# Performance work log

Measured on AMD Instinct MI355X. Metric: run time of the kernel, lower is better.

Reference implementation:

```python
import jax, jax.numpy as jnp
import numpy as np

N, E, DIN, DOUT = 10000, 160000, 256, 256
NEG_SLOPE = 0.2
BN_EPS = 1e-5
DROP_P = 0.5


def setup_inputs() -> dict:
    key = jax.random.key(0)
    ks = jax.random.split(key, 12)
    s = 1.0 / np.sqrt(DIN)
    return {
        "x": jax.random.normal(ks[0], (N, DIN), jnp.float32),
        "edge_index": jax.random.randint(ks[1], (2, E), 0, N, jnp.int64),
        "Wl": jax.random.normal(ks[2], (DIN, DOUT), jnp.float32) * s,
        "bl": jax.random.normal(ks[3], (DOUT,), jnp.float32) * s,
        "Wr": jax.random.normal(ks[4], (DIN, DOUT), jnp.float32) * s,
        "br": jax.random.normal(ks[5], (DOUT,), jnp.float32) * s,
        "att": jax.random.normal(ks[6], (DOUT,), jnp.float32) * (1.0 / np.sqrt(DOUT)),
        "bias": jax.random.normal(ks[7], (DOUT,), jnp.float32) * 0.01,
        "gamma": jnp.ones((DOUT,), jnp.float32),
        "beta": jnp.zeros((DOUT,), jnp.float32),
        "dropout_u": jax.random.uniform(ks[8], (N, DOUT), jnp.float32),
    }


def reference(x, edge_index, Wl, bl, Wr, br, att, bias, gamma, beta, dropout_u):
    n = x.shape[0]
    # GATv2Conv (heads=1): separate source/target linear maps
    xl = x @ Wl + bl  # source features [N, DOUT]
    xr = x @ Wr + br  # target features [N, DOUT]
    # add self-loops (PyG default add_self_loops=True)
    loop = jnp.arange(n, dtype=edge_index.dtype)
    src = jnp.concatenate([edge_index[0], loop])  # [E+N]
    dst = jnp.concatenate([edge_index[1], loop])
    # GATv2 attention: e = att . LeakyReLU(xl_j + xr_i)
    h = jax.nn.leaky_relu(xl[src] + xr[dst], NEG_SLOPE)  # [E+N, DOUT]
    alpha = h @ att  # [E+N]
    # segment softmax over destination nodes
    amax = jax.ops.segment_max(alpha, dst, num_segments=n)
    alpha = jnp.exp(alpha - amax[dst])
    denom = jax.ops.segment_sum(alpha, dst, num_segments=n)
    alpha = alpha / denom[dst]
    # scatter-add aggregate of weighted source features
    out = jax.ops.segment_sum(xl[src] * alpha[:, None], dst, num_segments=n)
    out = out + bias
    # ReLU -> dropout(p=0.5, training) -> BatchNorm (training stats)
    out = jax.nn.relu(out)
    mask = (dropout_u >= DROP_P).astype(out.dtype) / (1.0 - DROP_P)
    out = out * mask
    mean = out.mean(axis=0)
    var = out.var(axis=0)  # biased, as BatchNorm uses for normalization
    out = gamma * (out - mean) * jax.lax.rsqrt(var + BN_EPS) + beta
    return out
```

## Files before the change

kernel.cpp:

```cpp
#include <hip/hip_runtime.h>
#include <hip/hip_bf16.h>
#include <math.h>

#define D 256
#define CAP 128
#define NEG_SLOPE 0.2f
#define BN_EPS 1e-5f

typedef __attribute__((ext_vector_type(8))) short bf16x8;
typedef __attribute__((ext_vector_type(8))) unsigned short ushort8;
typedef __attribute__((ext_vector_type(4))) float f32x4;

__device__ inline unsigned short f2bf(float f) {
    union { float f; unsigned u; } v; v.f = f;
    unsigned u = v.u;
    unsigned r = u + 0x7FFFu + ((u >> 16) & 1u);
    return (unsigned short)(r >> 16);
}
__device__ inline float bf2f(unsigned short u) {
    union { unsigned u; float f; } v; v.u = ((unsigned)u) << 16; return v.f;
}

__global__ void prep_kernel(const float* __restrict__ Wl, const float* __restrict__ Wr,
                            int* __restrict__ zero_base, int nzero,
                            unsigned short* __restrict__ Bt) {
    int b = blockIdx.x;
    if (b < 42) {
        int idx = b * 256 + threadIdx.x;
        if (idx < nzero) zero_base[idx] = 0;
    } else {
        int n = b - 42;
        int k = threadIdx.x;
        const float* W = (n < 256) ? Wl : Wr;
        int nn = n & 255;
        Bt[(size_t)n * 256 + k] = f2bf(W[(size_t)k * 256 + nn]);
    }
}

__global__ __launch_bounds__(256) void gemm_scatter_kernel(
    const float* __restrict__ X, const unsigned short* __restrict__ Bt,
    const float* __restrict__ bl, const float* __restrict__ br,
    const int* __restrict__ ei, int* __restrict__ counts, int* __restrict__ ssrc,
    unsigned short* __restrict__ xlbf, float* __restrict__ xr,
    int M, int E, int N, int ngemm)
{
    if ((int)blockIdx.x >= ngemm) {
        int e = (blockIdx.x - ngemm) * 256 + threadIdx.x;
        if (e < E + N) {
            int src, dst;
            if (e < E) { src = ei[e]; dst = ei[E + e]; }
            else       { src = dst = e - E; }
            int pos = atomicAdd(&counts[dst], 1);
            if (pos < CAP) ssrc[dst * CAP + pos] = src;
        }
        return;
    }

    __shared__ __align__(16) unsigned short As[64][136];
    __shared__ __align__(16) unsigned short Bs[64][136];

    const int tid = threadIdx.x;
    const int wave = tid >> 6, lane = tid & 63;
    const int m_l = lane & 15, quad = lane >> 4;
    const int row0 = (blockIdx.x >> 3) * 64;
    const int n0 = (blockIdx.x & 7) * 64;

    f32x4 acc[4] = {};

    for (int k0 = 0; k0 < 256; k0 += 128) {
        __syncthreads();
        #pragma unroll
        for (int i = 0; i < 4; i++) {
            int c = tid + i * 256;
            int r = c >> 4;
            int u = (c & 15) * 8;
            int grow = row0 + r;
            ushort8 av = {0, 0, 0, 0, 0, 0, 0, 0};
            if (grow < M) {
                float4 f0 = *(const float4*)(X + (size_t)grow * 256 + k0 + u);
                float4 f1 = *(const float4*)(X + (size_t)grow * 256 + k0 + u + 4);
                av[0] = f2bf(f0.x); av[1] = f2bf(f0.y);
                av[2] = f2bf(f0.z); av[3] = f2bf(f0.w);
                av[4] = f2bf(f1.x); av[5] = f2bf(f1.y);
                av[6] = f2bf(f1.z); av[7] = f2bf(f1.w);
            }
            *(ushort8*)&As[r][u] = av;
            *(ushort8*)&Bs[r][u] = *(const ushort8*)(Bt + (size_t)(n0 + r) * 256 + k0 + u);
        }
        __syncthreads();

        #pragma unroll
        for (int kk0 = 0; kk0 < 128; kk0 += 32) {
            bf16x8 a = *(const bf16x8*)&As[wave * 16 + m_l][kk0 + quad * 8];
            #pragma unroll
            for (int c = 0; c < 4; c++) {
                bf16x8 b = *(const bf16x8*)&Bs[c * 16 + m_l][kk0 + quad * 8];
                acc[c] = __builtin_amdgcn_mfma_f32_16x16x32_bf16(a, b, acc[c], 0, 0, 0);
            }
        }
    }

    const bool isl = (n0 < 256);
    #pragma unroll
    for (int c = 0; c < 4; c++) {
        int col = n0 + c * 16 + m_l;
        int cc = col & 255;
        float bv = isl ? bl[cc] : br[cc];
        #pragma unroll
        for (int r = 0; r < 4; r++) {
            int row = row0 + wave * 16 + quad * 4 + r;
            if (row < M) {
                float v = acc[c][r] + bv;
                if (isl) xlbf[(size_t)row * 256 + cc] = f2bf(v);
                else     xr[(size_t)row * 256 + cc] = v;
            }
        }
    }
}

__device__ inline float dot8leaky(const float* f, float4 bA, float4 bB,
                                  float4 aA, float4 aB) {
    float h, s = 0.f;
    h = f[0] + bA.x; h = (h > 0.f) ? h : NEG_SLOPE * h; s += h * aA.x;
    h = f[1] + bA.y; h = (h > 0.f) ? h : NEG_SLOPE * h; s += h * aA.y;
    h = f[2] + bA.z; h = (h > 0.f) ? h : NEG_SLOPE * h; s += h * aA.z;
    h = f[3] + bA.w; h = (h > 0.f) ? h : NEG_SLOPE * h; s += h * aA.w;
    h = f[4] + bB.x; h = (h > 0.f) ? h : NEG_SLOPE * h; s += h * aB.x;
    h = f[5] + bB.y; h = (h > 0.f) ? h : NEG_SLOPE * h; s += h * aB.y;
    h = f[6] + bB.z; h = (h > 0.f) ? h : NEG_SLOPE * h; s += h * aB.z;
    h = f[7] + bB.w; h = (h > 0.f) ? h : NEG_SLOPE * h; s += h * aB.w;
    return s;
}

__global__ __launch_bounds__(256) void node_kernel(
    const unsigned short* __restrict__ xlbf, const float* __restrict__ xr,
    const float* __restrict__ att, const float* __restrict__ bias,
    const float* __restrict__ du, const int* __restrict__ counts,
    const int* __restrict__ ssrc, float* __restrict__ out, int N)
{
    const int wave = threadIdx.x >> 6, lane = threadIdx.x & 63;
    const int i = blockIdx.x * 4 + wave;
    if (i >= N) return;
    const int hl = lane & 31;
    const int sid = lane >> 5;

    const float4 attA = ((const float4*)att)[hl * 2];
    const float4 attB = ((const float4*)att)[hl * 2 + 1];
    const float4 bA = ((const float4*)(xr + (size_t)i * D))[hl * 2];
    const float4 bB = ((const float4*)(xr + (size_t)i * D))[hl * 2 + 1];

    int cnt = counts[i];
    if (cnt > CAP) cnt = CAP;
    const int start = i * CAP, end = start + cnt;

    float m = -INFINITY, lsum = 0.f;
    float acc[8] = {0.f, 0.f, 0.f, 0.f, 0.f, 0.f, 0.f, 0.f};
    const ushort8 z8 = {0, 0, 0, 0, 0, 0, 0, 0};

    int e = start + sid;
    ushort8 p0, p1, p2, p3;
    p0 = (e     < end) ? *(const ushort8*)(xlbf + (size_t)ssrc[e]     * D + hl * 8) : z8;
    p1 = (e + 2 < end) ? *(const ushort8*)(xlbf + (size_t)ssrc[e + 2] * D + hl * 8) : z8;
    p2 = (e + 4 < end) ? *(const ushort8*)(xlbf + (size_t)ssrc[e + 4] * D + hl * 8) : z8;
    p3 = (e + 6 < end) ? *(const ushort8*)(xlbf + (size_t)ssrc[e + 6] * D + hl * 8) : z8;

    while (e < end) {
        ushort8 c0 = p0, c1 = p1, c2 = p2, c3 = p3;
        bool v1 = (e + 2 < end), v2 = (e + 4 < end), v3 = (e + 6 < end);
        int en = e + 8;
        p0 = (en     < end) ? *(const ushort8*)(xlbf + (size_t)ssrc[en]     * D + hl * 8) : z8;
        p1 = (en + 2 < end) ? *(const ushort8*)(xlbf + (size_t)ssrc[en + 2] * D + hl * 8) : z8;
        p2 = (en + 4 < end) ? *(const ushort8*)(xlbf + (size_t)ssrc[en + 4] * D + hl * 8) : z8;
        p3 = (en + 6 < end) ? *(const ushort8*)(xlbf + (size_t)ssrc[en + 6] * D + hl * 8) : z8;

        float f0[8], f1[8], f2[8], f3[8];
        #pragma unroll
        for (int k = 0; k < 8; k++) {
            f0[k] = bf2f(c0[k]); f1[k] = bf2f(c1[k]);
            f2[k] = bf2f(c2[k]); f3[k] = bf2f(c3[k]);
        }

        float s0 = dot8leaky(f0, bA, bB, attA, attB);
        float s1 = dot8leaky(f1, bA, bB, attA, attB);
        float s2 = dot8leaky(f2, bA, bB, attA, attB);
        float s3 = dot8leaky(f3, bA, bB, attA, attB);

        #pragma unroll
        for (int off = 1; off < 32; off <<= 1) {
            s0 += __shfl_xor(s0, off);
            s1 += __shfl_xor(s1, off);
            s2 += __shfl_xor(s2, off);
            s3 += __shfl_xor(s3, off);
        }
        if (!v1) s1 = -INFINITY;
        if (!v2) s2 = -INFINITY;
        if (!v3) s3 = -INFINITY;

        float mnew = fmaxf(fmaxf(m, fmaxf(s0, s1)), fmaxf(s2, s3));
        float sc = __expf(m - mnew);
        float e0e = __expf(s0 - mnew);
        float e1e = __expf(s1 - mnew);
        float e2e = __expf(s2 - mnew);
        float e3e = __expf(s3 - mnew);
        lsum = lsum * sc + e0e + e1e + e2e + e3e;
        #pragma unroll
        for (int k = 0; k < 8; k++) {
            acc[k] = acc[k] * sc + e0e * f0[k] + e1e * f1[k]
                                 + e2e * f2[k] + e3e * f3[k];
        }
        m = mnew;
        e = en;
    }

    {
        float mO = __shfl_xor(m, 32);
        float lO = __shfl_xor(lsum, 32);
        float accO[8];
        #pragma unroll
        for (int k = 0; k < 8; k++) accO[k] = __shfl_xor(acc[k], 32);
        float mn = fmaxf(m, mO);
        float wS = (m  == -INFINITY) ? 0.f : __expf(m - mn);
        float wO = (mO == -INFINITY) ? 0.f : __expf(mO - mn);
        lsum = lsum * wS + lO * wO;
        #pragma unroll
        for (int k = 0; k < 8; k++) acc[k] = acc[k] * wS + accO[k] * wO;
    }

    if (lane < 32) {
        float inv = 1.f / lsum;
        float4 biA = ((const float4*)bias)[hl * 2];
        float4 biB = ((const float4*)bias)[hl * 2 + 1];
        float4 uA = ((const float4*)(du + (size_t)i * D))[hl * 2];
        float4 uB = ((const float4*)(du + (size_t)i * D))[hl * 2 + 1];
        float4 oA, oB;
        oA.x = fmaxf(acc[0] * inv + biA.x, 0.f); oA.x = (uA.x >= 0.5f) ? 2.f * oA.x : 0.f;
        oA.y = fmaxf(acc[1] * inv + biA.y, 0.f); oA.y = (uA.y >= 0.5f) ? 2.f * oA.y : 0.f;
        oA.z = fmaxf(acc[2] * inv + biA.z, 0.f); oA.z = (uA.z >= 0.5f) ? 2.f * oA.z : 0.f;
        oA.w = fmaxf(acc[3] * inv + biA.w, 0.f); oA.w = (uA.w >= 0.5f) ? 2.f * oA.w : 0.f;
        oB.x = fmaxf(acc[4] * inv + biB.x, 0.f); oB.x = (uB.x >= 0.5f) ? 2.f * oB.x : 0.f;
        oB.y = fmaxf(acc[5] * inv + biB.y, 0.f); oB.y = (uB.y >= 0.5f) ? 2.f * oB.y : 0.f;
        oB.z = fmaxf(acc[6] * inv + biB.z, 0.f); oB.z = (uB.z >= 0.5f) ? 2.f * oB.z : 0.f;
        oB.w = fmaxf(acc[7] * inv + biB.w, 0.f); oB.w = (uB.w >= 0.5f) ? 2.f * oB.w : 0.f;
        ((float4*)(out + (size_t)i * D))[hl * 2] = oA;
        ((float4*)(out + (size_t)i * D))[hl * 2 + 1] = oB;
    }
}

__global__ void bn_reduce_kernel(const float* __restrict__ pre,
                                 float* __restrict__ colsum,
                                 float* __restrict__ colsumsq, int N) {
    int t = threadIdx.x;
    float s = 0.f, s2 = 0.f;
    for (int r = blockIdx.x; r < N; r += gridDim.x) {
        float v = pre[(size_t)r * D + t];
        s += v; s2 += v * v;
    }
    atomicAdd(&colsum[t], s);
    atomicAdd(&colsumsq[t], s2);
}

__global__ void bn_apply_kernel(float* __restrict__ out,
                                const float* __restrict__ colsum,
                                const float* __restrict__ colsumsq,
                                const float* __restrict__ gamma,
                                const float* __restrict__ beta, int N) {
    int idx4 = blockIdx.x * 256 + threadIdx.x;
    int t0 = (idx4 * 4) & (D - 1);
    float invN = 1.f / (float)N;
    float4 v = ((const float4*)out)[idx4];
    float4 o;
    #pragma unroll
    for (int j = 0; j < 4; j++) {
        float mean = colsum[t0 + j] * invN;
        float var = colsumsq[t0 + j] * invN - mean * mean;
        float r = rsqrtf(var + BN_EPS);
        float vv = (j == 0) ? v.x : (j == 1) ? v.y : (j == 2) ? v.z : v.w;
        float oo = gamma[t0 + j] * (vv - mean) * r + beta[t0 + j];
        if (j == 0) o.x = oo; else if (j == 1) o.y = oo; else if (j == 2) o.z = oo; else o.w = oo;
    }
    ((float4*)out)[idx4] = o;
}

extern "C" void kernel_launch(void* const* d_in, const int* in_sizes, int n_in,
                              void* d_out, int out_size, void* d_ws, size_t ws_size,
                              hipStream_t stream) {
    const float* x     = (const float*)d_in[0];
    const int*   ei    = (const int*)d_in[1];
    const float* Wl    = (const float*)d_in[2];
    const float* bl    = (const float*)d_in[3];
    const float* Wr    = (const float*)d_in[4];
    const float* br    = (const float*)d_in[5];
    const float* att   = (const float*)d_in[6];
    const float* bias  = (const float*)d_in[7];
    const float* gamma = (const float*)d_in[8];
    const float* beta  = (const float*)d_in[9];
    const float* du    = (const float*)d_in[10];

    const int N = in_sizes[0] / D;
    const int E = in_sizes[1] / 2;

    int* ws = (int*)d_ws;
    size_t off = 0;
    float* xr       = (float*)(ws + off); off += (size_t)N * D;
    unsigned short* xlbf = (unsigned short*)(ws + off); off += (size_t)N * D / 2;
    unsigned short* Bt   = (unsigned short*)(ws + off); off += 512 * 256 / 2;
    int*   ssrc     = ws + off;           off += (size_t)N * CAP;
    float* colsum   = (float*)(ws + off); off += D;
    float* colsumsq = (float*)(ws + off); off += D;
    int*   counts   = ws + off;           off += N;
    int nzero = 2 * D + N;

    prep_kernel<<<42 + 512, 256, 0, stream>>>(Wl, Wr, (int*)colsum, nzero, Bt);

    int nMtiles = (N + 63) / 64;
    int ngemm = nMtiles * 8;
    int nscat = (E + N + 255) / 256;
    gemm_scatter_kernel<<<ngemm + nscat, 256, 0, stream>>>(
        x, Bt, bl, br, ei, counts, ssrc, xlbf, xr, N, E, N, ngemm);

    node_kernel<<<(N + 3) / 4, 256, 0, stream>>>(
        xlbf, xr, att, bias, du, counts, ssrc, (float*)d_out, N);

    bn_reduce_kernel<<<256, 256, 0, stream>>>((const float*)d_out, colsum, colsumsq, N);
    bn_apply_kernel<<<(N * D / 4 + 255) / 256, 256, 0, stream>>>(
        (float*)d_out, colsum, colsumsq, gamma, beta, N);
}
```

Before: 167.6 us.

## Pre-convert X to swizzled bf16 and load GEMM tiles directly into LDS

```diff
diff --git a/kernel.cpp b/kernel.cpp
--- a/kernel.cpp
+++ b/kernel.cpp
@@ -21,24 +21,50 @@
     union { unsigned u; float f; } v; v.u = ((unsigned)u) << 16; return v.f;
 }
 
-__global__ void prep_kernel(const float* __restrict__ Wl, const float* __restrict__ Wr,
+__device__ __forceinline__ void gload16(const void* g, void* l) {
+    __builtin_amdgcn_global_load_lds(
+        (const __attribute__((address_space(1))) unsigned int*)g,
+        (__attribute__((address_space(3))) unsigned int*)l,
+        16, 0, 0);
+}
+
+__global__ void prep_kernel(const float* __restrict__ X,
+                            const float* __restrict__ Wl, const float* __restrict__ Wr,
                             int* __restrict__ zero_base, int nzero,
-                            unsigned short* __restrict__ Bt) {
+                            unsigned short* __restrict__ Bt,
+                            unsigned short* __restrict__ Xbf, int N) {
     int b = blockIdx.x;
     if (b < 42) {
         int idx = b * 256 + threadIdx.x;
         if (idx < nzero) zero_base[idx] = 0;
-    } else {
+    } else if (b < 42 + 512) {
         int n = b - 42;
         int k = threadIdx.x;
         const float* W = (n < 256) ? Wl : Wr;
         int nn = n & 255;
-        Bt[(size_t)n * 256 + k] = f2bf(W[(size_t)k * 256 + nn]);
+        int ks = k ^ ((n & 7) << 3);
+        Bt[(size_t)n * 256 + ks] = f2bf(W[(size_t)k * 256 + nn]);
+    } else {
+        int idx = (b - 554) * 256 + threadIdx.x;
+        int row = idx >> 5;
+        int k0 = (idx & 31) * 8;
+        int ks = k0 ^ ((row & 7) << 3);
+        ushort8 v = {0, 0, 0, 0, 0, 0, 0, 0};
+        if (row < N) {
+            const float* src = X + (size_t)row * 256 + k0;
+            float4 f0 = *(const float4*)(src);
+            float4 f1 = *(const float4*)(src + 4);
+            v[0] = f2bf(f0.x); v[1] = f2bf(f0.y);
+            v[2] = f2bf(f0.z); v[3] = f2bf(f0.w);
+            v[4] = f2bf(f1.x); v[5] = f2bf(f1.y);
+            v[6] = f2bf(f1.z); v[7] = f2bf(f1.w);
+        }
+        *(ushort8*)(Xbf + (size_t)row * 256 + ks) = v;
     }
 }
 
 __global__ __launch_bounds__(256) void gemm_scatter_kernel(
-    const float* __restrict__ X, const unsigned short* __restrict__ Bt,
+    const unsigned short* __restrict__ Xbf, const unsigned short* __restrict__ Bt,
     const float* __restrict__ bl, const float* __restrict__ br,
     const int* __restrict__ ei, int* __restrict__ counts, int* __restrict__ ssrc,
     unsigned short* __restrict__ xlbf, float* __restrict__ xr,
@@ -56,14 +82,15 @@
         return;
     }
 
-    __shared__ __align__(16) unsigned short As[64][136];
-    __shared__ __align__(16) unsigned short Bs[64][136];
+    __shared__ __align__(16) unsigned short As[64 * 128];
+    __shared__ __align__(16) unsigned short Bs[64 * 128];
 
     const int tid = threadIdx.x;
     const int wave = tid >> 6, lane = tid & 63;
     const int m_l = lane & 15, quad = lane >> 4;
     const int row0 = (blockIdx.x >> 3) * 64;
     const int n0 = (blockIdx.x & 7) * 64;
+    const int sw = (m_l & 7) << 3;
 
     f32x4 acc[4] = {};
 
@@ -71,30 +98,23 @@
         __syncthreads();
         #pragma unroll
         for (int i = 0; i < 4; i++) {
-            int c = tid + i * 256;
-            int r = c >> 4;
-            int u = (c & 15) * 8;
-            int grow = row0 + r;
-            ushort8 av = {0, 0, 0, 0, 0, 0, 0, 0};
-            if (grow < M) {
-                float4 f0 = *(const float4*)(X + (size_t)grow * 256 + k0 + u);
-                float4 f1 = *(const float4*)(X + (size_t)grow * 256 + k0 + u + 4);
-                av[0] = f2bf(f0.x); av[1] = f2bf(f0.y);
-                av[2] = f2bf(f0.z); av[3] = f2bf(f0.w);
-                av[4] = f2bf(f1.x); av[5] = f2bf(f1.y);
-                av[6] = f2bf(f1.z); av[7] = f2bf(f1.w);
-            }
-            *(ushort8*)&As[r][u] = av;
-            *(ushort8*)&Bs[r][u] = *(const ushort8*)(Bt + (size_t)(n0 + r) * 256 + k0 + u);
+            int L = (tid + i * 256) * 16;
+            int r = L >> 8;
+            int cb = L & 255;
+            gload16((const char*)Xbf + (size_t)(row0 + r) * 512 + (size_t)k0 * 2 + cb,
+                    (char*)As + L);
+            gload16((const char*)Bt + (size_t)(n0 + r) * 512 + (size_t)k0 * 2 + cb,
+                    (char*)Bs + L);
         }
         __syncthreads();
 
         #pragma unroll
         for (int kk0 = 0; kk0 < 128; kk0 += 32) {
-            bf16x8 a = *(const bf16x8*)&As[wave * 16 + m_l][kk0 + quad * 8];
+            int ka = (kk0 + quad * 8) ^ sw;
+            bf16x8 a = *(const bf16x8*)&As[(wave * 16 + m_l) * 128 + ka];
             #pragma unroll
             for (int c = 0; c < 4; c++) {
-                bf16x8 b = *(const bf16x8*)&Bs[c * 16 + m_l][kk0 + quad * 8];
+                bf16x8 b = *(const bf16x8*)&Bs[(c * 16 + m_l) * 128 + ka];
                 acc[c] = __builtin_amdgcn_mfma_f32_16x16x32_bf16(a, b, acc[c], 0, 0, 0);
             }
         }
@@ -298,11 +318,13 @@
 
     const int N = in_sizes[0] / D;
     const int E = in_sizes[1] / 2;
+    const int Mpad = (N + 63) & ~63;
 
     int* ws = (int*)d_ws;
     size_t off = 0;
     float* xr       = (float*)(ws + off); off += (size_t)N * D;
     unsigned short* xlbf = (unsigned short*)(ws + off); off += (size_t)N * D / 2;
+    unsigned short* Xbf  = (unsigned short*)(ws + off); off += (size_t)Mpad * D / 2;
     unsigned short* Bt   = (unsigned short*)(ws + off); off += 512 * 256 / 2;
     int*   ssrc     = ws + off;           off += (size_t)N * CAP;
     float* colsum   = (float*)(ws + off); off += D;
@@ -310,13 +332,15 @@
     int*   counts   = ws + off;           off += N;
     int nzero = 2 * D + N;
 
-    prep_kernel<<<42 + 512, 256, 0, stream>>>(Wl, Wr, (int*)colsum, nzero, Bt);
+    int nconv = (Mpad * 32) / 256;
+    prep_kernel<<<42 + 512 + nconv, 256, 0, stream>>>(
+        x, Wl, Wr, (int*)colsum, nzero, Bt, Xbf, N);
 
     int nMtiles = (N + 63) / 64;
     int ngemm = nMtiles * 8;
     int nscat = (E + N + 255) / 256;
     gemm_scatter_kernel<<<ngemm + nscat, 256, 0, stream>>>(
-        x, Bt, bl, br, ei, counts, ssrc, xlbf, xr, N, E, N, ngemm);
+        Xbf, Bt, bl, br, ei, counts, ssrc, xlbf, xr, N, E, N, ngemm);
 
     node_kernel<<<(N + 3) / 4, 256, 0, stream>>>(
         xlbf, xr, att, bias, du, counts, ssrc, (float*)d_out, N);
```

After: 160.9 us. 1.04x faster.
